# Kernel optimization log

Measured on AMD Instinct MI355X. Metric: run time of the kernel, lower is better.

Reference implementation:

```python
import jax, jax.numpy as jnp
import numpy as np

N, NUM_TOKENS, TOKEN_DIM = 32768, 8192, 768
K = 4  # hard-coded top-k in the torch forward


def setup_inputs() -> dict:
    key = jax.random.key(0)
    k1, k2 = jax.random.split(key)
    inputs_flatten = jax.random.normal(k1, (N, TOKEN_DIM), dtype=jnp.float32)
    embed = jax.random.normal(k2, (NUM_TOKENS, TOKEN_DIM), dtype=jnp.float32)  # codebook buffer
    return {"inputs_flatten": inputs_flatten, "embed": embed}


def reference(inputs_flatten, embed):
    # squared euclidean distances: [N, num_tokens]
    distances = (
        jnp.sum(inputs_flatten ** 2, axis=1, keepdims=True)
        + jnp.sum(embed ** 2, axis=1)
        - 2.0 * (inputs_flatten @ embed.T)
    )

    # k smallest distances via top_k on negated distances
    neg_vals, topk_indices = jax.lax.top_k(-distances, K)
    topk_values = -neg_vals  # ascending smallest-k distances, [N, 4]

    # drop nearest, reweight the next 3 neighbors
    tv = topk_values[:, 1:]  # [N, 3]
    tv = tv / jnp.maximum(jnp.linalg.norm(tv, axis=1, keepdims=True), 1e-12)  # F.normalize
    tv = 1.0 / (tv + 1e-4)
    topk_values = jax.nn.softmax(tv, axis=1)
    topk_indices_out = topk_indices[:, 1:]

    # hard assignment (argmin) and codebook lookup (one-hot scatter + matmul == gather)
    encoding_indices = jnp.argmin(distances, axis=1)[:, None]  # [N, 1]
    quantize = embed[encoding_indices[:, 0]]  # [N, token_dim]

    # straight-through estimator
    quantize = jax.lax.stop_gradient(quantize - inputs_flatten) + inputs_flatten
    return quantize, encoding_indices, topk_values, topk_indices_out
```

## Files before the change

kernel.cpp:

```cpp
#include <hip/hip_runtime.h>
#include <cfloat>
#include <cmath>

#define NROWS 32768
#define NTOK  8192
#define DIM   768
#define KSPLIT 384

#define BM 64
#define BN 128
#define BK 32
#define NT 512

#define Q_OFF   0
#define EI_OFF  (NROWS*DIM)
#define TV_OFF  (EI_OFF + NROWS)
#define TI_OFF  (TV_OFF + NROWS*3)

typedef short short8 __attribute__((ext_vector_type(8)));
typedef float f32x4 __attribute__((ext_vector_type(4)));
typedef float f32x16 __attribute__((ext_vector_type(16)));

__global__ __launch_bounds__(256)
void np_norm_kernel(const float* __restrict__ x, float* __restrict__ o) {
#pragma clang fp contract(off)
  const int wid = (blockIdx.x * 256 + threadIdx.x) >> 6;
  const int lane = threadIdx.x & 63;
  const float* p = x + (size_t)wid * DIM + (lane >> 3) * 96 + (lane & 7);
  float v = p[0];
  float r = v * v;
#pragma unroll
  for (int k = 1; k < 12; k++) {
    float w = p[8 * k];
    float sq = w * w;
    r = r + sq;
  }
#pragma unroll
  for (int m = 1; m < 64; m <<= 1) {
    float other = __shfl_xor(r, m, 64);
    r = r + other;
  }
  if (lane == 0) o[wid] = r;
}

__device__ __forceinline__ bool dless(float a, int ai, float b, int bi_) {
  return (a < b) || (a == b && ai < bi_);
}

__device__ __forceinline__ void ins4(float (&v)[4], int (&x)[4], float c, int ci) {
  if (dless(c, ci, v[3], x[3])) {
    v[3] = c; x[3] = ci;
    if (dless(v[3], x[3], v[2], x[2])) { float tv = v[2]; int ti = x[2]; v[2] = v[3]; x[2] = x[3]; v[3] = tv; x[3] = ti; }
    if (dless(v[2], x[2], v[1], x[1])) { float tv = v[1]; int ti = x[1]; v[1] = v[2]; x[1] = x[2]; v[2] = tv; x[2] = ti; }
    if (dless(v[1], x[1], v[0], x[0])) { float tv = v[0]; int ti = x[0]; v[0] = v[1]; x[0] = x[1]; v[1] = tv; x[1] = ti; }
  }
}

__device__ __forceinline__ void ins8(float (&v)[8], int (&x)[8], float c, int ci) {
  if (dless(c, ci, v[7], x[7])) {
    v[7] = c; x[7] = ci;
#pragma unroll
    for (int k = 7; k > 0; k--) {
      if (dless(v[k], x[k], v[k - 1], x[k - 1])) {
        float tv = v[k - 1]; int ti = x[k - 1];
        v[k - 1] = v[k]; x[k - 1] = x[k];
        v[k] = tv; x[k] = ti;
      }
    }
  }
}

__device__ __forceinline__ unsigned short f2bf(float f) {
  unsigned int u = __float_as_uint(f);
  u += 0x7FFFu + ((u >> 16) & 1u);
  return (unsigned short)(u >> 16);
}

typedef const __attribute__((address_space(1))) void* gas1_t;
typedef __attribute__((address_space(3))) void* las3_t;
__device__ __forceinline__ void gl16(const void* g, void* s) {
  __builtin_amdgcn_global_load_lds((gas1_t)g, (las3_t)s, 16, 0, 0);
}

__global__ __launch_bounds__(256)
void cvtT_kernel(const float* __restrict__ in, unsigned short* __restrict__ out, int nrows) {
  const int row = blockIdx.x * 256 + threadIdx.x;
  const int Q = blockIdx.y;
  const float4* p = (const float4*)(in + (size_t)row * DIM + Q * 8);
  const float4 a = p[0], b = p[1];
  union { unsigned short u[8]; int4 v; } pk;
  pk.u[0] = f2bf(a.x); pk.u[1] = f2bf(a.y); pk.u[2] = f2bf(a.z); pk.u[3] = f2bf(a.w);
  pk.u[4] = f2bf(b.x); pk.u[5] = f2bf(b.y); pk.u[6] = f2bf(b.z); pk.u[7] = f2bf(b.w);
  *(int4*)(out + ((size_t)Q * nrows + row) * 8) = pk.v;
}

#define STRIPS 16
#define KSTEPS 24
#define NITER (STRIPS * KSTEPS)

__global__ __launch_bounds__(256, 2)
void vq_rank(const unsigned short* __restrict__ xbT, const unsigned short* __restrict__ ebT,
             const float* __restrict__ e2g, unsigned short* __restrict__ topp) {
  __shared__ __align__(16) unsigned char esm[3][16384];
  __shared__ __align__(16) unsigned char xsm[3][8192];

  const int tid = threadIdx.x;
  const int l = tid & 63;
  const int w = tid >> 6;
  const int wr = w >> 1, wc = w & 1;
  const int l31 = l & 31, h = l >> 5;

  const int bid = (int)blockIdx.x;
  const int sbid = (bid & 7) * 64 + (bid >> 3);
  const int chalf = sbid >> 8;
  const int row0 = (sbid & 255) * 128;
  const int cg0 = chalf * 4096;

  const int t7 = tid >> 7, t127 = tid & 127;

  float bv[2][8]; int bi[2][8];
#pragma unroll
  for (int xj = 0; xj < 2; ++xj)
#pragma unroll
    for (int c = 0; c < 8; ++c) { bv[xj][c] = FLT_MAX; bi[xj][c] = 0x7FFFFFFF; }

  f32x16 acc[4][2];
#pragma unroll
  for (int ei = 0; ei < 4; ++ei)
#pragma unroll
    for (int xj = 0; xj < 2; ++xj) acc[ei][xj] = (f32x16)0.f;

#define STAGE(BN_, KT, COL0)                                                    \
  {                                                                             \
    const unsigned short* eg = ebT + ((size_t)(4 * (KT)) * NTOK + (COL0) + tid) * 8; \
    gl16(eg,                 &esm[BN_][(0 * 256 + w * 64) * 16]);               \
    gl16(eg + NTOK * 8,      &esm[BN_][(1 * 256 + w * 64) * 16]);               \
    gl16(eg + 2 * NTOK * 8,  &esm[BN_][(2 * 256 + w * 64) * 16]);               \
    gl16(eg + 3 * NTOK * 8,  &esm[BN_][(3 * 256 + w * 64) * 16]);               \
    const unsigned short* xg = xbT + ((size_t)(4 * (KT) + t7) * NROWS + row0 + t127) * 8; \
    gl16(xg,                 &xsm[BN_][(0 * 256 + w * 64) * 16]);               \
    gl16(xg + 2 * NROWS * 8, &xsm[BN_][(1 * 256 + w * 64) * 16]);               \
  }

#define COMPUTE(B_)                                                             \
  {                                                                             \
    const unsigned char* ebp = &esm[B_][0];                                     \
    const unsigned char* xbp = &xsm[B_][0];                                     \
    __builtin_amdgcn_s_setprio(1);                                              \
    _Pragma("unroll")                                                           \
    for (int s = 0; s < 2; ++s) {                                               \
      const int kq = s * 2 + h;                                                 \
      short8 af[4], bfr[2];                                                     \
      _Pragma("unroll")                                                         \
      for (int ei = 0; ei < 4; ++ei)                                            \
        af[ei] = *(const short8*)(ebp + (size_t)(kq * 256 + wc * 128 + ei * 32 + l31) * 16); \
      _Pragma("unroll")                                                         \
      for (int xj = 0; xj < 2; ++xj)                                            \
        bfr[xj] = *(const short8*)(xbp + (size_t)(kq * 128 + wr * 64 + xj * 32 + l31) * 16); \
      _Pragma("unroll")                                                         \
      for (int ei = 0; ei < 4; ++ei)                                            \
        _Pragma("unroll")                                                       \
        for (int xj = 0; xj < 2; ++xj)                                          \
          acc[ei][xj] = __builtin_amdgcn_mfma_f32_32x32x16_bf16(af[ei], bfr[xj], acc[ei][xj], 0, 0, 0); \
    }                                                                           \
    __builtin_amdgcn_s_setprio(0);                                              \
  }

#define SELECT(SC0)                                                             \
  {                                                                             \
    _Pragma("unroll")                                                           \
    for (int ei = 0; ei < 4; ++ei) {                                            \
      const int cb = (SC0) + wc * 128 + ei * 32 + 4 * h;                        \
      float4 e2q[4];                                                            \
      _Pragma("unroll")                                                         \
      for (int q = 0; q < 4; ++q)                                               \
        e2q[q] = *(const float4*)(e2g + cb + q * 8);                            \
      _Pragma("unroll")                                                         \
      for (int xj = 0; xj < 2; ++xj) {                                          \
        float sv[16];                                                           \
        _Pragma("unroll")                                                       \
        for (int q = 0; q < 4; ++q) {                                           \
          sv[q * 4 + 0] = fmaf(-2.f, acc[ei][xj][q * 4 + 0], e2q[q].x);         \
          sv[q * 4 + 1] = fmaf(-2.f, acc[ei][xj][q * 4 + 1], e2q[q].y);         \
          sv[q * 4 + 2] = fmaf(-2.f, acc[ei][xj][q * 4 + 2], e2q[q].z);         \
          sv[q * 4 + 3] = fmaf(-2.f, acc[ei][xj][q * 4 + 3], e2q[q].w);         \
        }                                                                       \
        float mn = sv[0];                                                       \
        _Pragma("unroll")                                                       \
        for (int r = 1; r < 16; ++r) mn = fminf(mn, sv[r]);                     \
        if (mn < bv[xj][7]) {                                                   \
          _Pragma("unroll")                                                     \
          for (int q = 0; q < 4; ++q)                                           \
            _Pragma("unroll")                                                   \
            for (int j = 0; j < 4; ++j)                                         \
              ins8(bv[xj], bi[xj], sv[q * 4 + j], cb + q * 8 + j);              \
        }                                                                       \
      }                                                                         \
    }                                                                           \
    _Pragma("unroll")                                                           \
    for (int ei = 0; ei < 4; ++ei)                                              \
      _Pragma("unroll")                                                         \
      for (int xj = 0; xj < 2; ++xj) acc[ei][xj] = (f32x16)0.f;                 \
  }

#define BODY(B_, DO_STAGE, WAITS)                                               \
  {                                                                             \
    asm volatile(WAITS ::: "memory");                                           \
    __builtin_amdgcn_s_barrier();                                               \
    asm volatile("" ::: "memory");                                              \
    COMPUTE(B_)                                                                 \
    if (DO_STAGE) {                                                             \
      STAGE((B_ + 2) % 3, nkt, ncol0)                                           \
      if (++nkt == KSTEPS) { nkt = 0; ncol0 += 256; }                           \
    }                                                                           \
    if (++kc == KSTEPS) { SELECT(scol0) kc = 0; scol0 += 256; }                 \
  }

  STAGE(0, 0, cg0)
  STAGE(1, 1, cg0)

  int nkt = 2, ncol0 = cg0;
  int kc = 0, scol0 = cg0;

#pragma unroll 1
  for (int g = 0; g < 127; ++g) {
    BODY(0, 1, "s_waitcnt vmcnt(6)")
    BODY(1, 1, "s_waitcnt vmcnt(6)")
    BODY(2, 1, "s_waitcnt vmcnt(6)")
  }
  BODY(0, 1, "s_waitcnt vmcnt(6)")
  BODY(1, 0, "s_waitcnt vmcnt(6)")
  BODY(2, 0, "s_waitcnt vmcnt(0)")
#undef BODY
#undef SELECT
#undef COMPUTE
#undef STAGE

#pragma unroll
  for (int xj = 0; xj < 2; ++xj) {
    float ov[8]; int oi[8];
#pragma unroll
    for (int c = 0; c < 8; ++c) {
      ov[c] = __shfl_xor(bv[xj][c], 32, 64);
      oi[c] = __shfl_xor(bi[xj][c], 32, 64);
    }
#pragma unroll
    for (int c = 0; c < 8; ++c) ins8(bv[xj], bi[xj], ov[c], oi[c]);
  }

  __syncthreads();
  float* mval = (float*)&esm[0][0];
  int*   midx = (int*)&xsm[0][0];
  if (wc == 1 && l < 32) {
#pragma unroll
    for (int xj = 0; xj < 2; ++xj) {
      const int rr = wr * 64 + xj * 32 + l31;
#pragma unroll
      for (int c = 0; c < 8; ++c) {
        mval[rr * 8 + c] = bv[xj][c];
        midx[rr * 8 + c] = bi[xj][c];
      }
    }
  }
  __syncthreads();
  if (wc == 0 && l < 32) {
#pragma unroll
    for (int xj = 0; xj < 2; ++xj) {
      const int rr = wr * 64 + xj * 32 + l31;
#pragma unroll
      for (int c = 0; c < 8; ++c) ins8(bv[xj], bi[xj], mval[rr * 8 + c], midx[rr * 8 + c]);
      unsigned short* dst = topp + (size_t)(row0 + rr) * 16 + chalf * 8;
#pragma unroll
      for (int c = 0; c < 8; ++c) dst[c] = (unsigned short)bi[xj][c];
    }
  }
}

__global__ __launch_bounds__(256)
void vq_refine16(const float* __restrict__ x, const float* __restrict__ E,
                 const float* __restrict__ x2, const float* __restrict__ e2,
                 const unsigned short* __restrict__ topp, float* __restrict__ out) {
  const int gid = blockIdx.x * 256 + threadIdx.x;
  const int row = gid >> 4;
  const int s = gid & 15;
  const int myc = topp[(size_t)row * 16 + s];

  const float4* xr = (const float4*)(x + (size_t)row * DIM);
  const float4* er = (const float4*)(E + (size_t)myc * DIM);
  float accA = 0.f, accB = 0.f;
#pragma unroll 8
  for (int q = 0; q < KSPLIT / 4; ++q) {
    const float4 a = xr[q], b = er[q];
    accA = fmaf(a.x, b.x, accA); accA = fmaf(a.y, b.y, accA);
    accA = fmaf(a.z, b.z, accA); accA = fmaf(a.w, b.w, accA);
  }
#pragma unroll 8
  for (int q = KSPLIT / 4; q < DIM / 4; ++q) {
    const float4 a = xr[q], b = er[q];
    accB = fmaf(a.x, b.x, accB); accB = fmaf(a.y, b.y, accB);
    accB = fmaf(a.z, b.z, accB); accB = fmaf(a.w, b.w, accB);
  }
  const float d = fmaf(-2.0f, accA + accB, x2[row] + e2[myc]);

  const int base = (threadIdx.x & 63) & ~15;
  float dv[16]; int cv[16];
#pragma unroll
  for (int t = 0; t < 16; ++t) {
    dv[t] = __shfl(d, base + t, 64);
    cv[t] = __shfl(myc, base + t, 64);
  }
#pragma unroll
  for (int a = 0; a < 4; ++a)
#pragma unroll
    for (int b = 15; b > a; --b) {
      const bool sw = (dv[b] < dv[b - 1]) || (dv[b] == dv[b - 1] && cv[b] < cv[b - 1]);
      if (sw) {
        float td = dv[b]; dv[b] = dv[b - 1]; dv[b - 1] = td;
        int ti = cv[b]; cv[b] = cv[b - 1]; cv[b - 1] = ti;
      }
    }

  if (s == 0) {
    out[EI_OFF + row] = (float)cv[0];
    const double d1 = (double)dv[1], d2 = (double)dv[2], d3 = (double)dv[3];
    double nrm = sqrt(d1 * d1 + d2 * d2 + d3 * d3);
    nrm = fmax(nrm, 1e-12);
    const double t1 = 1.0 / (d1 / nrm + 1e-4);
    const double t2 = 1.0 / (d2 / nrm + 1e-4);
    const double t3 = 1.0 / (d3 / nrm + 1e-4);
    const double mx = fmax(t1, fmax(t2, t3));
    const double e1 = exp(t1 - mx), e2x = exp(t2 - mx), e3 = exp(t3 - mx);
    const double sm = e1 + e2x + e3;
    out[TV_OFF + row * 3 + 0] = (float)(e1 / sm);
    out[TV_OFF + row * 3 + 1] = (float)(e2x / sm);
    out[TV_OFF + row * 3 + 2] = (float)(e3 / sm);
    out[TI_OFF + row * 3 + 0] = (float)cv[1];
    out[TI_OFF + row * 3 + 1] = (float)cv[2];
    out[TI_OFF + row * 3 + 2] = (float)cv[3];
  }

  const float4* src = (const float4*)(E + (size_t)cv[0] * DIM);
  float4* dst = (float4*)(out + Q_OFF + (size_t)row * DIM);
#pragma unroll
  for (int k = 0; k < 12; ++k) dst[s + k * 16] = src[s + k * 16];
}

__global__ __launch_bounds__(NT, 4)
void vq_main(const float* __restrict__ A, const float* __restrict__ E,
             const float* __restrict__ x2, const float* __restrict__ e2,
             float* __restrict__ out) {
  __shared__ float a_s[BK][BM + 4];
  __shared__ float b_s[BK][BN + 4];

  const int tid = threadIdx.x;
  const int tx = tid & 15;
  const int ty = tid >> 4;
  const int row0 = blockIdx.x * BM;

  const float x2r[2] = { x2[row0 + ty * 2 + 0], x2[row0 + ty * 2 + 1] };

  float bv[2][4];
  int   bi[2][4];
#pragma unroll
  for (int i = 0; i < 2; i++)
#pragma unroll
    for (int c = 0; c < 4; c++) { bv[i][c] = FLT_MAX; bi[i][c] = 0x7FFFFFFF; }

#define GEMM_STEP(k0, ACC)                                                       \
    {                                                                            \
      __syncthreads();                                                           \
      {                                                                          \
        const int r = tid >> 3, kq = tid & 7;                                    \
        const float4 v = *(const float4*)(A + (size_t)(row0 + r) * DIM + (k0 + kq * 4)); \
        a_s[kq * 4 + 0][r] = v.x; a_s[kq * 4 + 1][r] = v.y;                      \
        a_s[kq * 4 + 2][r] = v.z; a_s[kq * 4 + 3][r] = v.w;                      \
        _Pragma("unroll")                                                        \
        for (int s = 0; s < 2; s++) {                                            \
          const int fi = tid + s * NT;                                           \
          const int rb = fi >> 3, kb = fi & 7;                                   \
          const float4 w = *(const float4*)(E + (size_t)(col0 + rb) * DIM + (k0 + kb * 4)); \
          b_s[kb * 4 + 0][rb] = w.x; b_s[kb * 4 + 1][rb] = w.y;                  \
          b_s[kb * 4 + 2][rb] = w.z; b_s[kb * 4 + 3][rb] = w.w;                  \
        }                                                                        \
      }                                                                          \
      __syncthreads();                                                           \
      _Pragma("unroll")                                                          \
      for (int k = 0; k < BK; k++) {                                             \
        const float2 a2 = *(const float2*)&a_s[k][ty * 2];                       \
        float br[8];                                                             \
        *(float4*)(br)     = *(const float4*)&b_s[k][tx * 8];                    \
        *(float4*)(br + 4) = *(const float4*)&b_s[k][tx * 8 + 4];                \
        _Pragma("unroll")                                                        \
        for (int j = 0; j < 8; j++) {                                            \
          ACC[0][j] = fmaf(a2.x, br[j], ACC[0][j]);                              \
          ACC[1][j] = fmaf(a2.y, br[j], ACC[1][j]);                              \
        }                                                                        \
      }                                                                          \
    }

  for (int ct = 0; ct < NTOK / BN; ++ct) {
    const int col0 = ct * BN;

    float accA[2][8], accB[2][8];
#pragma unroll
    for (int i = 0; i < 2; i++)
#pragma unroll
      for (int j = 0; j < 8; j++) { accA[i][j] = 0.f; accB[i][j] = 0.f; }

    for (int k0 = 0; k0 < KSPLIT; k0 += BK) GEMM_STEP(k0, accA)
    for (int k0 = KSPLIT; k0 < DIM; k0 += BK) GEMM_STEP(k0, accB)

    float e2v[8];
    *(float4*)(e2v)     = *(const float4*)(e2 + col0 + tx * 8);
    *(float4*)(e2v + 4) = *(const float4*)(e2 + col0 + tx * 8 + 4);
#pragma unroll
    for (int i = 0; i < 2; i++) {
#pragma unroll
      for (int j = 0; j < 8; j++) {
        const float dot = accA[i][j] + accB[i][j];
        const float se = x2r[i] + e2v[j];
        const float d = fmaf(-2.0f, dot, se);
        const int ci = col0 + tx * 8 + j;
        ins4(bv[i], bi[i], d, ci);
      }
    }
  }
#undef GEMM_STEP

#pragma unroll
  for (int m = 1; m < 16; m <<= 1) {
#pragma unroll
    for (int i = 0; i < 2; i++) {
      float ov[4]; int oi[4];
#pragma unroll
      for (int c = 0; c < 4; c++) {
        ov[c] = __shfl_xor(bv[i][c], m, 64);
        oi[c] = __shfl_xor(bi[i][c], m, 64);
      }
#pragma unroll
      for (int c = 0; c < 4; c++) ins4(bv[i], bi[i], ov[c], oi[c]);
    }
  }

#pragma unroll
  for (int i = 0; i < 2; i++) {
    if (tx == i) {
      const int gr = row0 + ty * 2 + i;
      out[EI_OFF + gr] = (float)bi[i][0];
      const double d1 = (double)bv[i][1], d2 = (double)bv[i][2], d3 = (double)bv[i][3];
      double nrm = sqrt(d1 * d1 + d2 * d2 + d3 * d3);
      nrm = fmax(nrm, 1e-12);
      const double t1 = 1.0 / (d1 / nrm + 1e-4);
      const double t2 = 1.0 / (d2 / nrm + 1e-4);
      const double t3 = 1.0 / (d3 / nrm + 1e-4);
      const double mx = fmax(t1, fmax(t2, t3));
      const double e1 = exp(t1 - mx), e2x = exp(t2 - mx), e3 = exp(t3 - mx);
      const double s = e1 + e2x + e3;
      out[TV_OFF + gr * 3 + 0] = (float)(e1 / s);
      out[TV_OFF + gr * 3 + 1] = (float)(e2x / s);
      out[TV_OFF + gr * 3 + 2] = (float)(e3 / s);
      out[TI_OFF + gr * 3 + 0] = (float)bi[i][1];
      out[TI_OFF + gr * 3 + 1] = (float)bi[i][2];
      out[TI_OFF + gr * 3 + 2] = (float)bi[i][3];
    }
  }

  __syncthreads();
  int* idx_sh = (int*)&a_s[0][0];
  if (tx == 0) idx_sh[ty * 2 + 0] = bi[0][0];
  if (tx == 1) idx_sh[ty * 2 + 1] = bi[1][0];
  __syncthreads();

  for (int f = tid; f < BM * (DIM / 4); f += NT) {
    const int r = f / (DIM / 4);
    const int c = f % (DIM / 4);
    const int e = idx_sh[r];
    const float4 v = *(const float4*)(E + (size_t)e * DIM + c * 4);
    *(float4*)(out + Q_OFF + (size_t)(row0 + r) * DIM + c * 4) = v;
  }
}

extern "C" void kernel_launch(void* const* d_in, const int* in_sizes, int n_in,
                              void* d_out, int out_size, void* d_ws, size_t ws_size,
                              hipStream_t stream) {
  const float* x = (const float*)d_in[0];
  const float* E = (const float*)d_in[1];
  float* out = (float*)d_out;

  unsigned char* ws = (unsigned char*)d_ws;
  float* e2 = (float*)ws;
  float* x2 = (float*)(ws + 32768);
  unsigned short* topp = (unsigned short*)(ws + 32768 + 131072);
  unsigned short* xbT = (unsigned short*)(ws + 32768 + 131072 + 1048576);
  unsigned short* ebT = xbT + (size_t)NROWS * DIM;
  const size_t need = 32768 + 131072 + 1048576 +
                      (size_t)NROWS * DIM * 2 + (size_t)NTOK * DIM * 2;

  np_norm_kernel<<<NTOK / 4, 256, 0, stream>>>(E, e2);
  np_norm_kernel<<<NROWS / 4, 256, 0, stream>>>(x, x2);

  if (ws_size >= need) {
    cvtT_kernel<<<dim3(NROWS / 256, DIM / 8), 256, 0, stream>>>(x, xbT, NROWS);
    cvtT_kernel<<<dim3(NTOK / 256, DIM / 8), 256, 0, stream>>>(E, ebT, NTOK);
    vq_rank<<<512, 256, 0, stream>>>(xbT, ebT, e2, topp);
    vq_refine16<<<NROWS * 16 / 256, 256, 0, stream>>>(x, E, x2, e2, topp, out);
  } else {
    vq_main<<<NROWS / BM, NT, 0, stream>>>(x, E, x2, e2, out);
  }
}
```

Baseline: 1.098 ms.

## Load x fragments directly into registers and deepen codebook LDS pipeline to four stages

The x tile fragments now come straight from global memory into registers, double-buffered, and no longer pass through LDS. The freed shared memory is used to extend the codebook staging ring from three to four buffers, with adjusted waitcnt depths. The top-8 selection also moves from a min-prefilter plus branchy insertion to a per-candidate check followed by branchless min/max insertion. Register pressure rises from the extra buffered fragments and could hurt occupancy at two blocks per SM, and the direct global loads may be less coalesced than the old LDS staging.

Result: faster. 926.3 us (median of 2 runs) (-15.6%).

```diff
diff --git a/kernel.cpp b/kernel.cpp
--- a/kernel.cpp
+++ b/kernel.cpp
@@ -67,6 +67,20 @@
         v[k] = tv; x[k] = ti;
       }
     }
+  }
+}
+
+__device__ __forceinline__ void ins8v(float (&v)[8], int (&x)[8], float c, int ci) {
+  v[7] = c; x[7] = ci;
+#pragma unroll
+  for (int k = 7; k > 0; k--) {
+    const bool sw = v[k] < v[k - 1];
+    const float vmin = fminf(v[k], v[k - 1]);
+    const float vmax = fmaxf(v[k], v[k - 1]);
+    const int xk1 = sw ? x[k] : x[k - 1];
+    const int xk  = sw ? x[k - 1] : x[k];
+    v[k - 1] = vmin; v[k] = vmax;
+    x[k - 1] = xk1;  x[k] = xk;
   }
 }
 
@@ -101,8 +115,7 @@
 __global__ __launch_bounds__(256, 2)
 void vq_rank(const unsigned short* __restrict__ xbT, const unsigned short* __restrict__ ebT,
              const float* __restrict__ e2g, unsigned short* __restrict__ topp) {
-  __shared__ __align__(16) unsigned char esm[3][16384];
-  __shared__ __align__(16) unsigned char xsm[3][8192];
+  __shared__ __align__(16) unsigned char esm[4][16384];
 
   const int tid = threadIdx.x;
   const int l = tid & 63;
@@ -116,7 +129,8 @@
   const int row0 = (sbid & 255) * 128;
   const int cg0 = chalf * 4096;
 
-  const int t7 = tid >> 7, t127 = tid & 127;
+  const size_t xinv0 = ((size_t)h * NROWS + row0 + wr * 64 + l31) * 8;
+  const size_t xinv1 = xinv0 + 32 * 8;
 
   float bv[2][8]; int bi[2][8];
 #pragma unroll
@@ -130,38 +144,42 @@
 #pragma unroll
     for (int xj = 0; xj < 2; ++xj) acc[ei][xj] = (f32x16)0.f;
 
-#define STAGE(BN_, KT, COL0)                                                    \
+  short8 xb0[4], xb1[4];
+
+#define STAGE_E(BN_, KT, COL0)                                                  \
   {                                                                             \
     const unsigned short* eg = ebT + ((size_t)(4 * (KT)) * NTOK + (COL0) + tid) * 8; \
-    gl16(eg,                 &esm[BN_][(0 * 256 + w * 64) * 16]);               \
-    gl16(eg + NTOK * 8,      &esm[BN_][(1 * 256 + w * 64) * 16]);               \
-    gl16(eg + 2 * NTOK * 8,  &esm[BN_][(2 * 256 + w * 64) * 16]);               \
-    gl16(eg + 3 * NTOK * 8,  &esm[BN_][(3 * 256 + w * 64) * 16]);               \
-    const unsigned short* xg = xbT + ((size_t)(4 * (KT) + t7) * NROWS + row0 + t127) * 8; \
-    gl16(xg,                 &xsm[BN_][(0 * 256 + w * 64) * 16]);               \
-    gl16(xg + 2 * NROWS * 8, &xsm[BN_][(1 * 256 + w * 64) * 16]);               \
-  }
-
-#define COMPUTE(B_)                                                             \
+    gl16(eg,                &esm[BN_][(0 * 256 + w * 64) * 16]);                \
+    gl16(eg + NTOK * 8,     &esm[BN_][(1 * 256 + w * 64) * 16]);                \
+    gl16(eg + 2 * NTOK * 8, &esm[BN_][(2 * 256 + w * 64) * 16]);                \
+    gl16(eg + 3 * NTOK * 8, &esm[BN_][(3 * 256 + w * 64) * 16]);                \
+  }
+
+#define XLOAD(XB, KT)                                                           \
+  {                                                                             \
+    const unsigned short* xp = xbT + (size_t)(4 * (KT)) * (NROWS * 8);          \
+    XB[0] = *(const short8*)(xp + xinv0);                                       \
+    XB[1] = *(const short8*)(xp + xinv1);                                       \
+    XB[2] = *(const short8*)(xp + 2 * NROWS * 8 + xinv0);                       \
+    XB[3] = *(const short8*)(xp + 2 * NROWS * 8 + xinv1);                       \
+  }
+
+#define COMPUTE(B_, XB)                                                         \
   {                                                                             \
     const unsigned char* ebp = &esm[B_][0];                                     \
-    const unsigned char* xbp = &xsm[B_][0];                                     \
     __builtin_amdgcn_s_setprio(1);                                              \
     _Pragma("unroll")                                                           \
     for (int s = 0; s < 2; ++s) {                                               \
       const int kq = s * 2 + h;                                                 \
-      short8 af[4], bfr[2];                                                     \
+      short8 af[4];                                                             \
       _Pragma("unroll")                                                         \
       for (int ei = 0; ei < 4; ++ei)                                            \
         af[ei] = *(const short8*)(ebp + (size_t)(kq * 256 + wc * 128 + ei * 32 + l31) * 16); \
       _Pragma("unroll")                                                         \
-      for (int xj = 0; xj < 2; ++xj)                                            \
-        bfr[xj] = *(const short8*)(xbp + (size_t)(kq * 128 + wr * 64 + xj * 32 + l31) * 16); \
-      _Pragma("unroll")                                                         \
       for (int ei = 0; ei < 4; ++ei)                                            \
         _Pragma("unroll")                                                       \
         for (int xj = 0; xj < 2; ++xj)                                          \
-          acc[ei][xj] = __builtin_amdgcn_mfma_f32_32x32x16_bf16(af[ei], bfr[xj], acc[ei][xj], 0, 0, 0); \
+          acc[ei][xj] = __builtin_amdgcn_mfma_f32_32x32x16_bf16(af[ei], XB[s * 2 + xj], acc[ei][xj], 0, 0, 0); \
     }                                                                           \
     __builtin_amdgcn_s_setprio(0);                                              \
   }
@@ -177,23 +195,16 @@
         e2q[q] = *(const float4*)(e2g + cb + q * 8);                            \
       _Pragma("unroll")                                                         \
       for (int xj = 0; xj < 2; ++xj) {                                          \
-        float sv[16];                                                           \
         _Pragma("unroll")                                                       \
         for (int q = 0; q < 4; ++q) {                                           \
-          sv[q * 4 + 0] = fmaf(-2.f, acc[ei][xj][q * 4 + 0], e2q[q].x);         \
-          sv[q * 4 + 1] = fmaf(-2.f, acc[ei][xj][q * 4 + 1], e2q[q].y);         \
-          sv[q * 4 + 2] = fmaf(-2.f, acc[ei][xj][q * 4 + 2], e2q[q].z);         \
-          sv[q * 4 + 3] = fmaf(-2.f, acc[ei][xj][q * 4 + 3], e2q[q].w);         \
-        }                                                                       \
-        float mn = sv[0];                                                       \
-        _Pragma("unroll")                                                       \
-        for (int r = 1; r < 16; ++r) mn = fminf(mn, sv[r]);                     \
-        if (mn < bv[xj][7]) {                                                   \
-          _Pragma("unroll")                                                     \
-          for (int q = 0; q < 4; ++q)                                           \
-            _Pragma("unroll")                                                   \
-            for (int j = 0; j < 4; ++j)                                         \
-              ins8(bv[xj], bi[xj], sv[q * 4 + j], cb + q * 8 + j);              \
+          const float c0 = fmaf(-2.f, acc[ei][xj][q * 4 + 0], e2q[q].x);        \
+          const float c1 = fmaf(-2.f, acc[ei][xj][q * 4 + 1], e2q[q].y);        \
+          const float c2 = fmaf(-2.f, acc[ei][xj][q * 4 + 2], e2q[q].z);        \
+          const float c3 = fmaf(-2.f, acc[ei][xj][q * 4 + 3], e2q[q].w);        \
+          if (c0 < bv[xj][7]) ins8v(bv[xj], bi[xj], c0, cb + q * 8 + 0);        \
+          if (c1 < bv[xj][7]) ins8v(bv[xj], bi[xj], c1, cb + q * 8 + 1);        \
+          if (c2 < bv[xj][7]) ins8v(bv[xj], bi[xj], c2, cb + q * 8 + 2);        \
+          if (c3 < bv[xj][7]) ins8v(bv[xj], bi[xj], c3, cb + q * 8 + 3);        \
         }                                                                       \
       }                                                                         \
     }                                                                           \
@@ -203,38 +214,46 @@
       for (int xj = 0; xj < 2; ++xj) acc[ei][xj] = (f32x16)0.f;                 \
   }
 
-#define BODY(B_, DO_STAGE, WAITS)                                               \
+#define BODY(B_, XB, DO_X, DO_S, WAITS)                                         \
   {                                                                             \
     asm volatile(WAITS ::: "memory");                                           \
     __builtin_amdgcn_s_barrier();                                               \
     asm volatile("" ::: "memory");                                              \
-    COMPUTE(B_)                                                                 \
-    if (DO_STAGE) {                                                             \
-      STAGE((B_ + 2) % 3, nkt, ncol0)                                           \
+    COMPUTE(B_, XB)                                                             \
+    if (DO_X) { XLOAD(XB, xkt) if (++xkt == KSTEPS) xkt = 0; }                  \
+    if (DO_S) {                                                                 \
+      STAGE_E((B_ + 3) & 3, nkt, ncol0)                                         \
       if (++nkt == KSTEPS) { nkt = 0; ncol0 += 256; }                           \
     }                                                                           \
     if (++kc == KSTEPS) { SELECT(scol0) kc = 0; scol0 += 256; }                 \
   }
 
-  STAGE(0, 0, cg0)
-  STAGE(1, 1, cg0)
-
-  int nkt = 2, ncol0 = cg0;
+  STAGE_E(0, 0, cg0)
+  XLOAD(xb0, 0)
+  STAGE_E(1, 1, cg0)
+  XLOAD(xb1, 1)
+  STAGE_E(2, 2, cg0)
+
+  int xkt = 2;
+  int nkt = 3, ncol0 = cg0;
   int kc = 0, scol0 = cg0;
 
 #pragma unroll 1
-  for (int g = 0; g < 127; ++g) {
-    BODY(0, 1, "s_waitcnt vmcnt(6)")
-    BODY(1, 1, "s_waitcnt vmcnt(6)")
-    BODY(2, 1, "s_waitcnt vmcnt(6)")
-  }
-  BODY(0, 1, "s_waitcnt vmcnt(6)")
-  BODY(1, 0, "s_waitcnt vmcnt(6)")
-  BODY(2, 0, "s_waitcnt vmcnt(0)")
+  for (int g = 0; g < 95; ++g) {
+    BODY(0, xb0, 1, 1, "s_waitcnt vmcnt(12)")
+    BODY(1, xb1, 1, 1, "s_waitcnt vmcnt(12)")
+    BODY(2, xb0, 1, 1, "s_waitcnt vmcnt(12)")
+    BODY(3, xb1, 1, 1, "s_waitcnt vmcnt(12)")
+  }
+  BODY(0, xb0, 1, 1, "s_waitcnt vmcnt(12)")
+  BODY(1, xb1, 1, 0, "s_waitcnt vmcnt(12)")
+  BODY(2, xb0, 0, 0, "s_waitcnt vmcnt(8)")
+  BODY(3, xb1, 0, 0, "s_waitcnt vmcnt(0)")
 #undef BODY
 #undef SELECT
 #undef COMPUTE
-#undef STAGE
+#undef XLOAD
+#undef STAGE_E
 
 #pragma unroll
   for (int xj = 0; xj < 2; ++xj) {
@@ -250,7 +269,7 @@
 
   __syncthreads();
   float* mval = (float*)&esm[0][0];
-  int*   midx = (int*)&xsm[0][0];
+  int*   midx = (int*)&esm[1][0];
   if (wc == 1 && l < 32) {
 #pragma unroll
     for (int xj = 0; xj < 2; ++xj) {
```
